# Kernel tuning notes

Hardware: AMD Instinct MI355X
Metric: run time of the kernel (lower is better)

The kernel has to match this reference:

```python
import jax, jax.numpy as jnp
import numpy as np

N_NODES = 50000
N_EDGES = 1600000
IN_DIM = 128
OUT_DIM = 128
NUM_HEADS = 4
HEAD_DIM = OUT_DIM // NUM_HEADS


def setup_inputs() -> dict:
    key = jax.random.key(0)
    ks = jax.random.split(key, 10)
    s_in = 1.0 / np.sqrt(IN_DIM)
    s_out = 1.0 / np.sqrt(OUT_DIM)
    return {
        "x": jax.random.normal(ks[0], (N_NODES, IN_DIM), dtype=jnp.float32),
        "edge_index": jax.random.randint(ks[1], (2, N_EDGES), 0, N_NODES, dtype=jnp.int64),
        "Wq": jax.random.uniform(ks[2], (OUT_DIM, IN_DIM), jnp.float32, -s_in, s_in),
        "bq": jax.random.uniform(ks[3], (OUT_DIM,), jnp.float32, -s_in, s_in),
        "Wk": jax.random.uniform(ks[4], (OUT_DIM, IN_DIM), jnp.float32, -s_in, s_in),
        "bk": jax.random.uniform(ks[5], (OUT_DIM,), jnp.float32, -s_in, s_in),
        "Wv": jax.random.uniform(ks[6], (OUT_DIM, IN_DIM), jnp.float32, -s_in, s_in),
        "bv": jax.random.uniform(ks[7], (OUT_DIM,), jnp.float32, -s_in, s_in),
        "Wo": jax.random.uniform(ks[8], (OUT_DIM, OUT_DIM), jnp.float32, -s_out, s_out),
        "bo": jax.random.uniform(ks[9], (OUT_DIM,), jnp.float32, -s_out, s_out),
    }


def reference(x, edge_index, Wq, bq, Wk, bk, Wv, bv, Wo, bo):
    n = x.shape[0]
    # node-level projections -> [N, H, Hd]
    Q = (x @ Wq.T + bq).reshape(n, NUM_HEADS, HEAD_DIM)
    K = (x @ Wk.T + bk).reshape(n, NUM_HEADS, HEAD_DIM)
    V = (x @ Wv.T + bv).reshape(n, NUM_HEADS, HEAD_DIM)
    src, dst = edge_index[0], edge_index[1]
    # edge scores: [E, H]
    scores = (Q[dst] * K[src]).sum(-1) / np.sqrt(HEAD_DIM).astype(np.float32)
    # global-max shifted exp (faithful to original, which uses a single global max)
    scores_exp = jnp.exp(scores - scores.max())
    # per-dst normalization: [N, H]
    scores_sum = jax.ops.segment_sum(scores_exp, dst, num_segments=n)
    attention = scores_exp / (scores_sum[dst] + 1e-8)  # dropout in eval mode = identity
    # weighted aggregate of V[src] into dst: [N, H, Hd]
    messages = V[src] * attention[:, :, None]
    out = jax.ops.segment_sum(messages, dst, num_segments=n)
    out = out.reshape(n, OUT_DIM) @ Wo.T + bo
    return jax.nn.relu(out)
```

## Files before the change

### kernel.cpp

```cpp
#include <hip/hip_runtime.h>

#define N_NODES 50000
#define N_EDGES 1600000
#define DIM 128
#define M_PAD 50048
#define SCAN_NB ((N_NODES + 255) / 256)

#define OFF_WCATB  0UL
#define OFF_BCAT   98304UL
#define OFF_XB     99840UL
#define OFF_C      12912128UL
#define OFF_SRC    64112128UL
#define OFF_RANK   67312128UL
#define OFF_RS     70512128UL
#define OFF_CNT    70712136UL
#define OFF_BSUM   70912136UL
#define OFF_AGG    70913168UL

typedef __attribute__((ext_vector_type(8))) short short8;
typedef __attribute__((ext_vector_type(4))) float floatx4;
typedef __attribute__((ext_vector_type(2))) float fx2;

__device__ __forceinline__ unsigned bf16r(float f) {
    unsigned u = __float_as_uint(f);
    return (u + 0x7fffu + ((u >> 16) & 1u)) >> 16;
}
__device__ __forceinline__ unsigned pack2(float a, float b) {
    return bf16r(a) | (bf16r(b) << 16);
}
__device__ __forceinline__ float blo(unsigned v) { return __uint_as_float(v << 16); }
__device__ __forceinline__ float bhi(unsigned v) { return __uint_as_float(v & 0xffff0000u); }

#define CVT_NB 6250
#define ZERO_NB SCAN_NB
#define PREPW_NB 192
__global__ __launch_bounds__(256) void k_prep(const float* __restrict__ x,
                                              unsigned short* __restrict__ xb,
                                              int* __restrict__ counts,
                                              const float* __restrict__ Wq, const float* __restrict__ bq,
                                              const float* __restrict__ Wk, const float* __restrict__ bk,
                                              const float* __restrict__ Wv, const float* __restrict__ bv,
                                              unsigned short* __restrict__ Wcatb,
                                              float* __restrict__ bcat) {
    int bx = blockIdx.x, t = threadIdx.x;
    if (bx < CVT_NB) {
        int i = bx * 256 + t;
        if (i < N_NODES * DIM / 4) {
            float4 f = ((const float4*)x)[i];
            ushort4 o;
            o.x = (unsigned short)bf16r(f.x); o.y = (unsigned short)bf16r(f.y);
            o.z = (unsigned short)bf16r(f.z); o.w = (unsigned short)bf16r(f.w);
            ((ushort4*)xb)[i] = o;
        }
    } else if (bx < CVT_NB + ZERO_NB) {
        int i = (bx - CVT_NB) * 256 + t;
        if (i < N_NODES) counts[i] = 0;
    } else {
        int i = (bx - CVT_NB - ZERO_NB) * 256 + t;
        if (i < 3 * DIM * DIM) {
            int ro = i >> 7, col = i & 127;
            const float* W = (ro < 128) ? Wq : (ro < 256) ? Wk : Wv;
            Wcatb[i] = (unsigned short)bf16r(W[(ro & 127) * DIM + col]);
        }
        if (i < 3 * DIM) {
            const float* b = (i < 128) ? bq : (i < 256) ? bk : bv;
            bcat[i] = b[i & 127];
        }
    }
}

#define GQ_MB (M_PAD / 64)
#define GQ_BLOCKS (GQ_MB * 6)
#define HIST_NB 6250
#define GQH_GRID (1564 * 7)
__global__ __launch_bounds__(256) void k_gemmqkv_hist(const unsigned short* __restrict__ xb,
                                                      const unsigned short* __restrict__ Wb,
                                                      const float* __restrict__ bias,
                                                      unsigned* __restrict__ Cu, int M,
                                                      const int* __restrict__ dstA,
                                                      int* __restrict__ counts,
                                                      unsigned short* __restrict__ rank16) {
    __shared__ __align__(16) unsigned short As[64][136];
    __shared__ __align__(16) unsigned short Bs[64][136];
    const int grp = blockIdx.x / 7, r = blockIdx.x % 7;
    if (r >= 3) {
        int h = grp * 4 + (r - 3);
        if (h < HIST_NB) {
            int e = h * 256 + threadIdx.x;
            if (e < N_EDGES) rank16[e] = (unsigned short)atomicAdd(&counts[dstA[e]], 1);
        }
        return;
    }
    const int g = grp * 3 + r;
    const int m0 = (g % GQ_MB) * 64, n0 = (g / GQ_MB) * 64;
    const int t = threadIdx.x;
    {
        int row = t >> 2, ch = t & 3;
        const uint4* xrow = (const uint4*)(xb + (long)(m0 + row) * 128);
        const uint4* wrow = (const uint4*)(Wb + (long)(n0 + row) * 128);
#pragma unroll
        for (int j = 0; j < 4; ++j) {
            *(uint4*)&As[row][(ch + 4 * j) * 8] = xrow[ch + 4 * j];
            *(uint4*)&Bs[row][(ch + 4 * j) * 8] = wrow[ch + 4 * j];
        }
    }
    __syncthreads();
    const int w = t >> 6, lane = t & 63;
    const int quad = lane >> 4, c = lane & 15;
    floatx4 acc[4] = {{0.f,0.f,0.f,0.f},{0.f,0.f,0.f,0.f},{0.f,0.f,0.f,0.f},{0.f,0.f,0.f,0.f}};
#pragma unroll
    for (int ks = 0; ks < 4; ++ks) {
        short8 a = *(const short8*)&As[w * 16 + c][ks * 32 + quad * 8];
#pragma unroll
        for (int nt = 0; nt < 4; ++nt) {
            short8 b = *(const short8*)&Bs[nt * 16 + c][ks * 32 + quad * 8];
            acc[nt] = __builtin_amdgcn_mfma_f32_16x16x32_bf16(a, b, acc[nt], 0, 0, 0);
        }
    }
#pragma unroll
    for (int nt = 0; nt < 4; ++nt) {
        int gn = n0 + nt * 16 + c;
        float bv = bias[gn];
        int slice = gn >> 7;
        int cs = gn & 127;
#pragma unroll
        for (int i = 0; i < 4; ++i) {
            int gm = m0 + w * 16 + quad * 4 + i;
            float o = acc[nt][i] + bv;
            float f1 = __shfl_xor(o, 1);
            float f2 = __shfl_xor(o, 2);
            float f3 = __shfl_xor(o, 3);
            if (gm < M) {
                unsigned* crow = Cu + (long)gm * 256;
                if (slice == 0) {
                    ((float*)crow)[cs] = o;
                } else if (slice == 1) {
                    if ((c & 3) == 0) {
                        int pk = __builtin_amdgcn_cvt_pk_fp8_f32(o, f1, 0, false);
                        pk = __builtin_amdgcn_cvt_pk_fp8_f32(f2, f3, pk, true);
                        crow[128 + (cs >> 2)] = (unsigned)pk;
                    }
                } else {
                    if ((c & 1) == 0) crow[160 + (cs >> 1)] = pack2(o, f1);
                }
            }
        }
    }
}

__global__ __launch_bounds__(256) void k_scanA(const int* __restrict__ counts,
                                               int* __restrict__ bsum) {
    __shared__ int red[256];
    int t = threadIdx.x, i = blockIdx.x * 256 + t;
    red[t] = (i < N_NODES) ? counts[i] : 0;
    __syncthreads();
    for (int off = 128; off > 0; off >>= 1) {
        if (t < off) red[t] += red[t + off];
        __syncthreads();
    }
    if (t == 0) bsum[blockIdx.x] = red[0];
}
__global__ __launch_bounds__(256) void k_scanB(int* __restrict__ bsum, int nb) {
    __shared__ int s[256];
    int t = threadIdx.x;
    int v = (t < nb) ? bsum[t] : 0;
    s[t] = v;
    __syncthreads();
    for (int off = 1; off < 256; off <<= 1) {
        int u = (t >= off) ? s[t - off] : 0;
        __syncthreads();
        s[t] += u;
        __syncthreads();
    }
    if (t < nb) bsum[t] = s[t] - v;
}
__global__ __launch_bounds__(256) void k_scanC(const int* __restrict__ counts,
                                               const int* __restrict__ bsum,
                                               int* __restrict__ row_start) {
    __shared__ int s[256];
    int t = threadIdx.x, i = blockIdx.x * 256 + t;
    int v = (i < N_NODES) ? counts[i] : 0;
    s[t] = v;
    __syncthreads();
    for (int off = 1; off < 256; off <<= 1) {
        int u = (t >= off) ? s[t - off] : 0;
        __syncthreads();
        s[t] += u;
        __syncthreads();
    }
    int excl = bsum[blockIdx.x] + s[t] - v;
    if (i < N_NODES) {
        row_start[i] = excl;
        if (i == N_NODES - 1) row_start[N_NODES] = excl + v;
    }
}

__global__ void k_fill(const int* __restrict__ srcA, const int* __restrict__ dstA,
                       const int* __restrict__ row_start,
                       const unsigned short* __restrict__ rank16,
                       unsigned short* __restrict__ csr_src) {
    int e = blockIdx.x * blockDim.x + threadIdx.x;
    if (e < N_EDGES) {
        int d = dstA[e];
        csr_src[row_start[d] + rank16[e]] = (unsigned short)srcA[e];
    }
}

__global__ __launch_bounds__(256) void k_attn(const unsigned* __restrict__ Cu,
                                              const int* __restrict__ row_start,
                                              const unsigned short* __restrict__ csr_src,
                                              float* __restrict__ agg) {
    int d = blockIdx.x * 4 + (threadIdx.x >> 6);
    int lane = threadIdx.x & 63;
    if (d >= N_NODES) return;
    const int half = lane >> 5, sl = lane & 31;
    const float scale = 0.17677669529663687f;
    float4 q4 = *(const float4*)((const float*)(Cu + (long)d * 256) + 4 * sl);
    q4.x *= scale; q4.y *= scale; q4.z *= scale; q4.w *= scale;
    int s0 = row_start[d], s1 = row_start[d + 1];
    float lsum = 0.f, a0 = 0.f, a1 = 0.f, a2 = 0.f, a3 = 0.f;
    int pos = s0;
    for (; pos + 8 <= s1; pos += 8) {
        int base = pos + half * 4;
        int sa = csr_src[base + 0];
        int sb = csr_src[base + 1];
        int sc2 = csr_src[base + 2];
        int sd = csr_src[base + 3];
        const unsigned* ra = Cu + (long)sa * 256;
        const unsigned* rb = Cu + (long)sb * 256;
        const unsigned* rc = Cu + (long)sc2 * 256;
        const unsigned* rd = Cu + (long)sd * 256;
        unsigned ka = ra[128 + sl];
        unsigned kb = rb[128 + sl];
        unsigned kc = rc[128 + sl];
        unsigned kd = rd[128 + sl];
        uint2 va = *(const uint2*)(ra + 160 + 2 * sl);
        uint2 vb = *(const uint2*)(rb + 160 + 2 * sl);
        uint2 vc = *(const uint2*)(rc + 160 + 2 * sl);
        uint2 vd = *(const uint2*)(rd + 160 + 2 * sl);
        fx2 a01 = __builtin_amdgcn_cvt_pk_f32_fp8((int)ka, false);
        fx2 a23 = __builtin_amdgcn_cvt_pk_f32_fp8((int)ka, true);
        fx2 b01 = __builtin_amdgcn_cvt_pk_f32_fp8((int)kb, false);
        fx2 b23 = __builtin_amdgcn_cvt_pk_f32_fp8((int)kb, true);
        fx2 c01 = __builtin_amdgcn_cvt_pk_f32_fp8((int)kc, false);
        fx2 c23 = __builtin_amdgcn_cvt_pk_f32_fp8((int)kc, true);
        fx2 d01 = __builtin_amdgcn_cvt_pk_f32_fp8((int)kd, false);
        fx2 d23 = __builtin_amdgcn_cvt_pk_f32_fp8((int)kd, true);
        float pa = q4.x * a01.x + q4.y * a01.y + q4.z * a23.x + q4.w * a23.y;
        float pb = q4.x * b01.x + q4.y * b01.y + q4.z * b23.x + q4.w * b23.y;
        float pc = q4.x * c01.x + q4.y * c01.y + q4.z * c23.x + q4.w * c23.y;
        float pd = q4.x * d01.x + q4.y * d01.y + q4.z * d23.x + q4.w * d23.y;
        pa += __shfl_xor(pa, 1); pa += __shfl_xor(pa, 2); pa += __shfl_xor(pa, 4);
        pb += __shfl_xor(pb, 1); pb += __shfl_xor(pb, 2); pb += __shfl_xor(pb, 4);
        pc += __shfl_xor(pc, 1); pc += __shfl_xor(pc, 2); pc += __shfl_xor(pc, 4);
        pd += __shfl_xor(pd, 1); pd += __shfl_xor(pd, 2); pd += __shfl_xor(pd, 4);
        float wa = __expf(pa), wb = __expf(pb), wc = __expf(pc), wd = __expf(pd);
        lsum += (wa + wb) + (wc + wd);
        a0 += wa * blo(va.x) + wb * blo(vb.x) + wc * blo(vc.x) + wd * blo(vd.x);
        a1 += wa * bhi(va.x) + wb * bhi(vb.x) + wc * bhi(vc.x) + wd * bhi(vd.x);
        a2 += wa * blo(va.y) + wb * blo(vb.y) + wc * blo(vc.y) + wd * blo(vd.y);
        a3 += wa * bhi(va.y) + wb * bhi(vb.y) + wc * bhi(vc.y) + wd * bhi(vd.y);
    }
    for (; pos < s1; pos += 2) {
        int e = pos + half;
        bool ok = e < s1;
        int sa = csr_src[ok ? e : (s1 - 1)];
        const unsigned* ra = Cu + (long)sa * 256;
        unsigned ka = ra[128 + sl];
        uint2 va = *(const uint2*)(ra + 160 + 2 * sl);
        fx2 a01 = __builtin_amdgcn_cvt_pk_f32_fp8((int)ka, false);
        fx2 a23 = __builtin_amdgcn_cvt_pk_f32_fp8((int)ka, true);
        float pa = q4.x * a01.x + q4.y * a01.y + q4.z * a23.x + q4.w * a23.y;
        pa += __shfl_xor(pa, 1); pa += __shfl_xor(pa, 2); pa += __shfl_xor(pa, 4);
        float wa = ok ? __expf(pa) : 0.f;
        lsum += wa;
        a0 += wa * blo(va.x);
        a1 += wa * bhi(va.x);
        a2 += wa * blo(va.y);
        a3 += wa * bhi(va.y);
    }
    lsum += __shfl_xor(lsum, 32);
    a0 += __shfl_xor(a0, 32);
    a1 += __shfl_xor(a1, 32);
    a2 += __shfl_xor(a2, 32);
    a3 += __shfl_xor(a3, 32);
    if (lane < 32) {
        float inv = 1.f / (lsum + 1e-8f);
        float4 o;
        o.x = a0 * inv; o.y = a1 * inv; o.z = a2 * inv; o.w = a3 * inv;
        *(float4*)&agg[(long)d * 128 + 4 * sl] = o;
    }
}

__global__ __launch_bounds__(256) void k_gemm(const float* __restrict__ A,
                                              const float* __restrict__ B,
                                              const float* __restrict__ bias,
                                              float* __restrict__ Cp, int M) {
    __shared__ float As[32][64];
    __shared__ float Bs[32][64];
    const int m0 = blockIdx.x * 64, n0 = blockIdx.y * 64;
    const int t = threadIdx.x;
    const int tm = (t & 15) * 4, tn = (t >> 4) * 4;
    float acc[4][4] = {};
    for (int k0 = 0; k0 < 128; k0 += 32) {
#pragma unroll
        for (int i = 0; i < 2; ++i) {
            int idx = t + i * 256;
            int row = idx >> 3;
            int c4 = (idx & 7) * 4;
            float4 fa = make_float4(0.f, 0.f, 0.f, 0.f);
            if (m0 + row < M) fa = *(const float4*)&A[(long)(m0 + row) * 128 + k0 + c4];
            As[c4 + 0][row] = fa.x; As[c4 + 1][row] = fa.y;
            As[c4 + 2][row] = fa.z; As[c4 + 3][row] = fa.w;
            float4 fb = *(const float4*)&B[(long)(n0 + row) * 128 + k0 + c4];
            Bs[c4 + 0][row] = fb.x; Bs[c4 + 1][row] = fb.y;
            Bs[c4 + 2][row] = fb.z; Bs[c4 + 3][row] = fb.w;
        }
        __syncthreads();
#pragma unroll
        for (int k = 0; k < 32; ++k) {
            float4 a = *(const float4*)&As[k][tm];
            float4 b = *(const float4*)&Bs[k][tn];
            acc[0][0] += a.x * b.x; acc[0][1] += a.x * b.y; acc[0][2] += a.x * b.z; acc[0][3] += a.x * b.w;
            acc[1][0] += a.y * b.x; acc[1][1] += a.y * b.y; acc[1][2] += a.y * b.z; acc[1][3] += a.y * b.w;
            acc[2][0] += a.z * b.x; acc[2][1] += a.z * b.y; acc[2][2] += a.z * b.z; acc[2][3] += a.z * b.w;
            acc[3][0] += a.w * b.x; acc[3][1] += a.w * b.y; acc[3][2] += a.w * b.z; acc[3][3] += a.w * b.w;
        }
        __syncthreads();
    }
    float4 bv4 = *(const float4*)&bias[n0 + tn];
#pragma unroll
    for (int i = 0; i < 4; ++i) {
        int m = m0 + tm + i;
        if (m >= M) continue;
        float4 o;
        o.x = fmaxf(acc[i][0] + bv4.x, 0.f); o.y = fmaxf(acc[i][1] + bv4.y, 0.f);
        o.z = fmaxf(acc[i][2] + bv4.z, 0.f); o.w = fmaxf(acc[i][3] + bv4.w, 0.f);
        *(float4*)&Cp[(long)m * 128 + n0 + tn] = o;
    }
}

extern "C" void kernel_launch(void* const* d_in, const int* in_sizes, int n_in,
                              void* d_out, int out_size, void* d_ws, size_t ws_size,
                              hipStream_t stream) {
    const float* x  = (const float*)d_in[0];
    const int* edge = (const int*)d_in[1];
    const float* Wq = (const float*)d_in[2];
    const float* bq = (const float*)d_in[3];
    const float* Wk = (const float*)d_in[4];
    const float* bk = (const float*)d_in[5];
    const float* Wv = (const float*)d_in[6];
    const float* bv = (const float*)d_in[7];
    const float* Wo = (const float*)d_in[8];
    const float* bo = (const float*)d_in[9];
    float* out = (float*)d_out;

    char* ws = (char*)d_ws;
    unsigned short* Wcatb = (unsigned short*)(ws + OFF_WCATB);
    float* bcat      = (float*)(ws + OFF_BCAT);
    unsigned short* xb = (unsigned short*)(ws + OFF_XB);
    unsigned* Cu     = (unsigned*)(ws + OFF_C);
    unsigned short* csr_src = (unsigned short*)(ws + OFF_SRC);
    unsigned short* rank16  = (unsigned short*)(ws + OFF_RANK);
    int*   row_start = (int*)(ws + OFF_RS);
    int*   counts    = (int*)(ws + OFF_CNT);
    int*   bsum      = (int*)(ws + OFF_BSUM);
    float* agg       = (float*)(ws + OFF_AGG);

    const int* srcA = edge;
    const int* dstA = edge + N_EDGES;

    k_prep<<<CVT_NB + ZERO_NB + PREPW_NB, 256, 0, stream>>>(
        x, xb, counts, Wq, bq, Wk, bk, Wv, bv, Wcatb, bcat);

    k_gemmqkv_hist<<<GQH_GRID, 256, 0, stream>>>(
        xb, Wcatb, bcat, Cu, N_NODES, dstA, counts, rank16);

    k_scanA<<<SCAN_NB, 256, 0, stream>>>(counts, bsum);
    k_scanB<<<1, 256, 0, stream>>>(bsum, SCAN_NB);
    k_scanC<<<SCAN_NB, 256, 0, stream>>>(counts, bsum, row_start);
    k_fill<<<(N_EDGES + 255) / 256, 256, 0, stream>>>(srcA, dstA, row_start, rank16, csr_src);

    k_attn<<<(N_NODES + 3) / 4, 256, 0, stream>>>(Cu, row_start, csr_src, agg);

    k_gemm<<<dim3((N_NODES + 63) / 64, 2), 256, 0, stream>>>(agg, Wo, bo, out, N_NODES);
}
```

Before: 313.1 us.

## Build CSR with two-level bucketed counting sort instead of global atomics

Replaces the per-edge global atomic histogram, three-pass node scan and random scatter fill with a two-level counting sort. Edges are first bucketed by dst>>8 into 196 coarse buckets, using shared-memory histograms per chunk and a scan over the chunk-bucket counts. Each bucket is then sorted locally in shared memory to emit row_start and csr_src. The goal is to remove global atomic contention and scattered writes. The cost is an extra pass over a 4-byte bucketed array plus more kernel launches, and the final pass runs only 196 blocks.

```diff
diff --git a/kernel.cpp b/kernel.cpp
--- a/kernel.cpp
+++ b/kernel.cpp
@@ -4,18 +4,21 @@
 #define N_EDGES 1600000
 #define DIM 128
 #define M_PAD 50048
-#define SCAN_NB ((N_NODES + 255) / 256)
+#define NBKT 196
+#define CHUNK 6250
+#define BB 256
 
 #define OFF_WCATB  0UL
 #define OFF_BCAT   98304UL
 #define OFF_XB     99840UL
 #define OFF_C      12912128UL
 #define OFF_SRC    64112128UL
-#define OFF_RANK   67312128UL
-#define OFF_RS     70512128UL
-#define OFF_CNT    70712136UL
-#define OFF_BSUM   70912136UL
-#define OFF_AGG    70913168UL
+#define OFF_BKD    67312128UL
+#define OFF_CNT    73712128UL
+#define OFF_BSUM   73912832UL
+#define OFF_BOFF   73913664UL
+#define OFF_RS     73914496UL
+#define OFF_AGG    74114560UL
 
 typedef __attribute__((ext_vector_type(8))) short short8;
 typedef __attribute__((ext_vector_type(4))) float floatx4;
@@ -32,19 +35,29 @@
 __device__ __forceinline__ float bhi(unsigned v) { return __uint_as_float(v & 0xffff0000u); }
 
 #define CVT_NB 6250
-#define ZERO_NB SCAN_NB
 #define PREPW_NB 192
+#define PREP_GRID (BB + CVT_NB + PREPW_NB)
 __global__ __launch_bounds__(256) void k_prep(const float* __restrict__ x,
                                               unsigned short* __restrict__ xb,
-                                              int* __restrict__ counts,
                                               const float* __restrict__ Wq, const float* __restrict__ bq,
                                               const float* __restrict__ Wk, const float* __restrict__ bk,
                                               const float* __restrict__ Wv, const float* __restrict__ bv,
                                               unsigned short* __restrict__ Wcatb,
-                                              float* __restrict__ bcat) {
+                                              float* __restrict__ bcat,
+                                              const int* __restrict__ dstA,
+                                              int* __restrict__ cnt) {
+    __shared__ int h[NBKT];
     int bx = blockIdx.x, t = threadIdx.x;
-    if (bx < CVT_NB) {
-        int i = bx * 256 + t;
+    if (bx < BB) {
+        if (t < NBKT) h[t] = 0;
+        __syncthreads();
+        int base = bx * CHUNK;
+        for (int i = t; i < CHUNK; i += 256)
+            atomicAdd(&h[dstA[base + i] >> 8], 1);
+        __syncthreads();
+        if (t < NBKT) cnt[t * BB + bx] = h[t];
+    } else if (bx < BB + CVT_NB) {
+        int i = (bx - BB) * 256 + t;
         if (i < N_NODES * DIM / 4) {
             float4 f = ((const float4*)x)[i];
             ushort4 o;
@@ -52,11 +65,8 @@
             o.z = (unsigned short)bf16r(f.z); o.w = (unsigned short)bf16r(f.w);
             ((ushort4*)xb)[i] = o;
         }
-    } else if (bx < CVT_NB + ZERO_NB) {
-        int i = (bx - CVT_NB) * 256 + t;
-        if (i < N_NODES) counts[i] = 0;
     } else {
-        int i = (bx - CVT_NB - ZERO_NB) * 256 + t;
+        int i = (bx - BB - CVT_NB) * 256 + t;
         if (i < 3 * DIM * DIM) {
             int ro = i >> 7, col = i & 127;
             const float* W = (ro < 128) ? Wq : (ro < 256) ? Wk : Wv;
@@ -69,31 +79,81 @@
     }
 }
 
+__global__ __launch_bounds__(256) void k_b2a(const int* __restrict__ cnt, int* __restrict__ bsum) {
+    __shared__ int red[256];
+    int t = threadIdx.x;
+    red[t] = cnt[blockIdx.x * BB + t];
+    __syncthreads();
+    for (int off = 128; off > 0; off >>= 1) {
+        if (t < off) red[t] += red[t + off];
+        __syncthreads();
+    }
+    if (t == 0) bsum[blockIdx.x] = red[0];
+}
+__global__ __launch_bounds__(256) void k_b2b(const int* __restrict__ bsum, int* __restrict__ bktoff) {
+    __shared__ int s[256];
+    int t = threadIdx.x;
+    int v = (t < NBKT) ? bsum[t] : 0;
+    s[t] = v;
+    __syncthreads();
+    for (int off = 1; off < 256; off <<= 1) {
+        int u = (t >= off) ? s[t - off] : 0;
+        __syncthreads();
+        s[t] += u;
+        __syncthreads();
+    }
+    if (t < NBKT) bktoff[t] = s[t] - v;
+    if (t == NBKT - 1) bktoff[NBKT] = s[t];
+}
+__global__ __launch_bounds__(256) void k_b2c(int* __restrict__ cnt, const int* __restrict__ bktoff) {
+    __shared__ int s[256];
+    int t = threadIdx.x;
+    int v = cnt[blockIdx.x * BB + t];
+    s[t] = v;
+    __syncthreads();
+    for (int off = 1; off < 256; off <<= 1) {
+        int u = (t >= off) ? s[t - off] : 0;
+        __syncthreads();
+        s[t] += u;
+        __syncthreads();
+    }
+    cnt[blockIdx.x * BB + t] = bktoff[blockIdx.x] + s[t] - v;
+}
+
 #define GQ_MB (M_PAD / 64)
 #define GQ_BLOCKS (GQ_MB * 6)
-#define HIST_NB 6250
-#define GQH_GRID (1564 * 7)
-__global__ __launch_bounds__(256) void k_gemmqkv_hist(const unsigned short* __restrict__ xb,
-                                                      const unsigned short* __restrict__ Wb,
-                                                      const float* __restrict__ bias,
-                                                      unsigned* __restrict__ Cu, int M,
-                                                      const int* __restrict__ dstA,
-                                                      int* __restrict__ counts,
-                                                      unsigned short* __restrict__ rank16) {
+#define GB3_GRPS 261
+#define GB3_GRID (GB3_GRPS * 19)
+__global__ __launch_bounds__(256) void k_gemmqkv_b3(const unsigned short* __restrict__ xb,
+                                                    const unsigned short* __restrict__ Wb,
+                                                    const float* __restrict__ bias,
+                                                    unsigned* __restrict__ Cu, int M,
+                                                    const int* __restrict__ srcA,
+                                                    const int* __restrict__ dstA,
+                                                    const int* __restrict__ cnt,
+                                                    unsigned* __restrict__ bucketed) {
     __shared__ __align__(16) unsigned short As[64][136];
     __shared__ __align__(16) unsigned short Bs[64][136];
-    const int grp = blockIdx.x / 7, r = blockIdx.x % 7;
-    if (r >= 3) {
-        int h = grp * 4 + (r - 3);
-        if (h < HIST_NB) {
-            int e = h * 256 + threadIdx.x;
-            if (e < N_EDGES) rank16[e] = (unsigned short)atomicAdd(&counts[dstA[e]], 1);
+    __shared__ int cur[NBKT];
+    const int grp = blockIdx.x / 19, r = blockIdx.x % 19;
+    const int t = threadIdx.x;
+    if (r == 18) {
+        if (grp < BB) {
+            if (t < NBKT) cur[t] = cnt[t * BB + grp];
+            __syncthreads();
+            int base = grp * CHUNK;
+            for (int i = t; i < CHUNK; i += 256) {
+                int e = base + i;
+                int d = dstA[e];
+                int p = atomicAdd(&cur[d >> 8], 1);
+                bucketed[p] = (unsigned)srcA[e] | ((unsigned)(d & 255) << 16);
+            }
         }
         return;
     }
-    const int g = grp * 3 + r;
+    const int g = grp * 18 + r;
+    if (g >= GQ_BLOCKS) return;
     const int m0 = (g % GQ_MB) * 64, n0 = (g / GQ_MB) * 64;
-    const int t = threadIdx.x;
     {
         int row = t >> 2, ch = t & 3;
         const uint4* xrow = (const uint4*)(xb + (long)(m0 + row) * 128);
@@ -148,22 +208,19 @@
     }
 }
 
-__global__ __launch_bounds__(256) void k_scanA(const int* __restrict__ counts,
-                                               int* __restrict__ bsum) {
-    __shared__ int red[256];
-    int t = threadIdx.x, i = blockIdx.x * 256 + t;
-    red[t] = (i < N_NODES) ? counts[i] : 0;
-    __syncthreads();
-    for (int off = 128; off > 0; off >>= 1) {
-        if (t < off) red[t] += red[t + off];
-        __syncthreads();
-    }
-    if (t == 0) bsum[blockIdx.x] = red[0];
-}
-__global__ __launch_bounds__(256) void k_scanB(int* __restrict__ bsum, int nb) {
-    __shared__ int s[256];
-    int t = threadIdx.x;
-    int v = (t < nb) ? bsum[t] : 0;
+__global__ __launch_bounds__(256) void k_b4(const unsigned* __restrict__ bucketed,
+                                            const int* __restrict__ bktoff,
+                                            unsigned short* __restrict__ csr_src,
+                                            int* __restrict__ row_start) {
+    __shared__ int h[256], s[256], cur[256];
+    int b = blockIdx.x, t = threadIdx.x;
+    int base = bktoff[b], end = bktoff[b + 1];
+    h[t] = 0;
+    __syncthreads();
+    for (int p = base + t; p < end; p += 256)
+        atomicAdd(&h[bucketed[p] >> 16], 1);
+    __syncthreads();
+    int v = h[t];
     s[t] = v;
     __syncthreads();
     for (int off = 1; off < 256; off <<= 1) {
@@ -172,37 +229,16 @@
         s[t] += u;
         __syncthreads();
     }
-    if (t < nb) bsum[t] = s[t] - v;
-}
-__global__ __launch_bounds__(256) void k_scanC(const int* __restrict__ counts,
-                                               const int* __restrict__ bsum,
-                                               int* __restrict__ row_start) {
-    __shared__ int s[256];
-    int t = threadIdx.x, i = blockIdx.x * 256 + t;
-    int v = (i < N_NODES) ? counts[i] : 0;
-    s[t] = v;
-    __syncthreads();
-    for (int off = 1; off < 256; off <<= 1) {
-        int u = (t >= off) ? s[t - off] : 0;
-        __syncthreads();
-        s[t] += u;
-        __syncthreads();
-    }
-    int excl = bsum[blockIdx.x] + s[t] - v;
-    if (i < N_NODES) {
-        row_start[i] = excl;
-        if (i == N_NODES - 1) row_start[N_NODES] = excl + v;
-    }
-}
-
-__global__ void k_fill(const int* __restrict__ srcA, const int* __restrict__ dstA,
-                       const int* __restrict__ row_start,
-                       const unsigned short* __restrict__ rank16,
-                       unsigned short* __restrict__ csr_src) {
-    int e = blockIdx.x * blockDim.x + threadIdx.x;
-    if (e < N_EDGES) {
-        int d = dstA[e];
-        csr_src[row_start[d] + rank16[e]] = (unsigned short)srcA[e];
+    int start = base + s[t] - v;
+    int d = b * 256 + t;
+    if (d < N_NODES) row_start[d] = start;
+    if (d == N_NODES - 1) row_start[N_NODES] = N_EDGES;
+    cur[t] = start;
+    __syncthreads();
+    for (int p = base + t; p < end; p += 256) {
+        unsigned u = bucketed[p];
+        int q = atomicAdd(&cur[u >> 16], 1);
+        csr_src[q] = (unsigned short)(u & 0xffffu);
     }
 }
 
@@ -361,25 +397,27 @@
     unsigned short* xb = (unsigned short*)(ws + OFF_XB);
     unsigned* Cu     = (unsigned*)(ws + OFF_C);
     unsigned short* csr_src = (unsigned short*)(ws + OFF_SRC);
-    unsigned short* rank16  = (unsigned short*)(ws + OFF_RANK);
+    unsigned* bucketed = (unsigned*)(ws + OFF_BKD);
+    int*   cnt       = (int*)(ws + OFF_CNT);
+    int*   bsum      = (int*)(ws + OFF_BSUM);
+    int*   bktoff    = (int*)(ws + OFF_BOFF);
     int*   row_start = (int*)(ws + OFF_RS);
-    int*   counts    = (int*)(ws + OFF_CNT);
-    int*   bsum      = (int*)(ws + OFF_BSUM);
     float* agg       = (float*)(ws + OFF_AGG);
 
     const int* srcA = edge;
     const int* dstA = edge + N_EDGES;
 
-    k_prep<<<CVT_NB + ZERO_NB + PREPW_NB, 256, 0, stream>>>(
-        x, xb, counts, Wq, bq, Wk, bk, Wv, bv, Wcatb, bcat);
-
-    k_gemmqkv_hist<<<GQH_GRID, 256, 0, stream>>>(
-        xb, Wcatb, bcat, Cu, N_NODES, dstA, counts, rank16);
-
-    k_scanA<<<SCAN_NB, 256, 0, stream>>>(counts, bsum);
-    k_scanB<<<1, 256, 0, stream>>>(bsum, SCAN_NB);
-    k_scanC<<<SCAN_NB, 256, 0, stream>>>(counts, bsum, row_start);
-    k_fill<<<(N_EDGES + 255) / 256, 256, 0, stream>>>(srcA, dstA, row_start, rank16, csr_src);
+    k_prep<<<PREP_GRID, 256, 0, stream>>>(
+        x, xb, Wq, bq, Wk, bk, Wv, bv, Wcatb, bcat, dstA, cnt);
+
+    k_b2a<<<NBKT, 256, 0, stream>>>(cnt, bsum);
+    k_b2b<<<1, 256, 0, stream>>>(bsum, bktoff);
+    k_b2c<<<NBKT, 256, 0, stream>>>(cnt, bktoff);
+
+    k_gemmqkv_b3<<<GB3_GRID, 256, 0, stream>>>(
+        xb, Wcatb, bcat, Cu, N_NODES, srcA, dstA, cnt, bucketed);
+
+    k_b4<<<NBKT, 256, 0, stream>>>(bucketed, bktoff, csr_src, row_start);
 
     k_attn<<<(N_NODES + 3) / 4, 256, 0, stream>>>(Cu, row_start, csr_src, agg);
 
```

After: 287.0 us. 1.09x faster.
